# Performance work log

Measured on AMD Instinct MI355X. Metric: run time of the kernel, lower is better.

Reference implementation:

```python
import jax, jax.numpy as jnp
import numpy as np

B_, L, S_IN, S_OUT, Z_IN, Z_OUT = 2, 768, 1280, 32, 1, 32
D_INNER, D_STATE, D_CONV, DT_RANK = 64, 16, 4, 2  # expand=2 -> d_inner=64; dt_rank=ceil(32/16)=2


def setup_inputs() -> dict:
    key = jax.random.key(0)
    ks = jax.random.split(key, 12)
    p = lambda i, shape, scale=0.02: jax.random.normal(ks[i], shape, jnp.float32) * scale
    return dict(
        s=jax.random.normal(ks[0], (B_, L, S_IN), jnp.float32),
        z=jax.random.normal(ks[1], (B_, L, L, Z_IN), jnp.float32),
        s_proj_w=p(2, (S_OUT, S_IN)), s_proj_b=jnp.zeros((S_OUT,), jnp.float32),
        z_proj_w=p(3, (Z_OUT, Z_IN)), z_proj_b=jnp.zeros((Z_OUT,), jnp.float32),
        in_proj_w=p(4, (2 * D_INNER, S_OUT)),
        conv_w=p(5, (D_INNER, D_CONV)), conv_b=jnp.zeros((D_INNER,), jnp.float32),
        x_proj_w=p(6, (DT_RANK + 2 * D_STATE, D_INNER)),
        dt_proj_w=p(7, (D_INNER, DT_RANK)), dt_proj_b=p(8, (D_INNER,), 1.0),
        A_log=jnp.log(jnp.broadcast_to(jnp.arange(1, D_STATE + 1, dtype=jnp.float32), (D_INNER, D_STATE))),
        D=jnp.ones((D_INNER,), jnp.float32),
        out_proj_w=p(9, (S_OUT, D_INNER)),
    )


def mamba(u, in_proj_w, conv_w, conv_b, x_proj_w, dt_proj_w, dt_proj_b, A_log, D, out_proj_w):
    # u: [b, l, d_model]
    b, l, _ = u.shape
    xz = u @ in_proj_w.T                      # [b, l, 2*d_inner]
    x, gate = jnp.split(xz, 2, axis=-1)
    # causal depthwise conv1d, kernel D_CONV, then SiLU
    xp = jnp.pad(x, ((0, 0), (D_CONV - 1, 0), (0, 0)))
    x = sum(xp[:, k:k + l, :] * conv_w[:, k] for k in range(D_CONV)) + conv_b
    x = jax.nn.silu(x)
    x_dbl = x @ x_proj_w.T                    # [b, l, dt_rank + 2*d_state]
    dt, Bm, Cm = jnp.split(x_dbl, [DT_RANK, DT_RANK + D_STATE], axis=-1)
    dt = jax.nn.softplus(dt @ dt_proj_w.T + dt_proj_b)   # [b, l, d_inner]
    A = -jnp.exp(A_log)                       # [d_inner, d_state]
    dA = jnp.exp(dt[..., None] * A)           # [b, l, d, n]
    dBu = dt[..., None] * Bm[:, :, None, :] * x[..., None]  # [b, l, d, n]

    def step(h, ins):
        dA_t, dBu_t, C_t = ins
        h = dA_t * h + dBu_t                  # [b, d, n]
        return h, jnp.einsum('bdn,bn->bd', h, C_t)

    h0 = jnp.zeros((b, D_INNER, D_STATE), u.dtype)
    _, ys = jax.lax.scan(step, h0, (jnp.swapaxes(dA, 0, 1), jnp.swapaxes(dBu, 0, 1), jnp.swapaxes(Cm, 0, 1)))
    y = jnp.swapaxes(ys, 0, 1) + x * D        # D skip connection
    y = y * jax.nn.silu(gate)                 # gated output
    return y @ out_proj_w.T                   # [b, l, d_model]


def reference(s, z, s_proj_w, s_proj_b, z_proj_w, z_proj_b, in_proj_w, conv_w, conv_b,
              x_proj_w, dt_proj_w, dt_proj_b, A_log, D, out_proj_w):
    s_prime = s @ s_proj_w.T + s_proj_b                       # [b, l, 32]
    s_prime = mamba(s_prime, in_proj_w, conv_w, conv_b, x_proj_w,
                    dt_proj_w, dt_proj_b, A_log, D, out_proj_w)
    z_prime = z @ z_proj_w.T + z_proj_b                       # [b, l, l, 32]
    z_prime = z_prime + jnp.einsum('bsf,btf->bstf', s_prime, s_prime)
    return (s_prime, z_prime)
```

## Files before the change

### kernel.cpp

```cpp
#include <hip/hip_runtime.h>
#include <math.h>

#define B_     2
#define L_     768
#define SIN_   1280
#define SOUT_  32
#define DI_    64
#define DST_   16
#define DCONV_ 4
#define DTR_   2
#define NCH    48
#define CH     16


__global__ __launch_bounds__(256) void k_sproj(
    const float* __restrict__ s, const float* __restrict__ spw,
    const float* __restrict__ spb, const float* __restrict__ ipw,
    float* __restrict__ xz)
{
    __shared__ float srow[4][SIN_];
    __shared__ float w2[128 * 33];
    __shared__ float u[4][SOUT_];
    const int tid = threadIdx.x;
    const int row0 = blockIdx.x * 4;

    for (int r = 0; r < 4; ++r) {
        const float4* src = (const float4*)(s + (long)(row0 + r) * SIN_);
        for (int i = tid; i < SIN_ / 4; i += 256)
            ((float4*)srow[r])[i] = src[i];
    }
    for (int i = tid; i < 128 * 32; i += 256)
        w2[(i >> 5) * 33 + (i & 31)] = ipw[i];
    __syncthreads();

    const int f = tid >> 3;
    const int c = tid & 7;
    float p0 = 0.f, p1 = 0.f, p2 = 0.f, p3 = 0.f;
    const float* wrow = spw + (long)f * SIN_;
    for (int k = c; k < SIN_; k += 8) {
        float w = wrow[k];
        p0 += srow[0][k] * w; p1 += srow[1][k] * w;
        p2 += srow[2][k] * w; p3 += srow[3][k] * w;
    }
    #pragma unroll
    for (int m = 1; m <= 4; m <<= 1) {
        p0 += __shfl_xor(p0, m); p1 += __shfl_xor(p1, m);
        p2 += __shfl_xor(p2, m); p3 += __shfl_xor(p3, m);
    }
    if (c == 0) {
        float b = spb[f];
        u[0][f] = p0 + b; u[1][f] = p1 + b;
        u[2][f] = p2 + b; u[3][f] = p3 + b;
    }
    __syncthreads();

    const int j  = tid & 127;
    const int rh = tid >> 7;
    #pragma unroll
    for (int rp = 0; rp < 2; ++rp) {
        int r = rp * 2 + rh;
        float acc = 0.f;
        const float* wj = &w2[j * 33];
        #pragma unroll
        for (int k = 0; k < SOUT_; ++k) acc += u[r][k] * wj[k];
        xz[(long)(row0 + r) * 128 + j] = acc;
    }
}

__global__ __launch_bounds__(256) void k_pre(
    const float* __restrict__ xz, const float* __restrict__ convw,
    const float* __restrict__ convb, const float* __restrict__ xpw,
    const float* __restrict__ dtw, const float* __restrict__ dtb,
    float* __restrict__ xs_out, float* __restrict__ dtf,
    float* __restrict__ dtx, float* __restrict__ Bws, float* __restrict__ Cws)
{
    const int row0 = blockIdx.x * 4;
    const int tid = threadIdx.x;
    const int r = tid >> 6, d = tid & 63;
    const int row = row0 + r;
    const int b = row / L_, l = row - b * L_;
    __shared__ float sxpw[64][34];
    __shared__ float sdtw[128];
    __shared__ float sxs[4][DI_];
    __shared__ float sxd[4][34];

    for (int i = tid; i < 34 * 64; i += 256) {
        int j = i >> 6, k = i & 63;
        sxpw[k][j] = xpw[i];
    }
    if (tid < 128) sdtw[tid] = dtw[tid];

    float xc = convb[d];
    #pragma unroll
    for (int k = 0; k < DCONV_; ++k) {
        int ls = l + k - (DCONV_ - 1);
        if (ls >= 0) xc = fmaf(xz[(long)(b * L_ + ls) * 128 + d], convw[d * 4 + k], xc);
    }
    float xsv = xc / (1.f + expf(-xc));
    sxs[r][d] = xsv;
    xs_out[(long)row * DI_ + d] = xsv;
    __syncthreads();

    if (d < DTR_ + 2 * DST_) {
        float acc = 0.f;
        #pragma unroll
        for (int k = 0; k < 64; ++k) acc = fmaf(sxs[r][k], sxpw[k][d], acc);
        sxd[r][d] = acc;
    }
    __syncthreads();

    if (d < DST_) {
        Bws[(long)row * DST_ + d] = sxd[r][DTR_ + d];
        Cws[(long)row * DST_ + d] = sxd[r][DTR_ + DST_ + d];
    }
    float dtv = fmaf(sxd[r][0], sdtw[d * 2], fmaf(sxd[r][1], sdtw[d * 2 + 1], dtb[d]));
    dtv = dtv > 20.f ? dtv : log1pf(expf(dtv));
    dtf[(long)row * DI_ + d] = dtv;
    dtx[(long)row * DI_ + d] = dtv * xsv;
}

__global__ __launch_bounds__(256) void k_scan_p1(
    const float* __restrict__ dtf, const float* __restrict__ dtx,
    const float* __restrict__ Bws, const float* __restrict__ Alog,
    float* __restrict__ Pst, float* __restrict__ Lst)
{
    const int blk = blockIdx.x;
    const int dq  = blk & 3;
    const int bc  = blk >> 2;
    const int b   = bc / NCH, c = bc - b * NCH;
    const int tid = threadIdx.x;
    const int dl  = tid >> 4, n = tid & 15;
    const int d   = dq * 16 + dl;
    const long base = (long)b * L_ + c * CH;

    __shared__ float sB[CH][16];
    __shared__ float sdt[CH][16];
    __shared__ float sdx[CH][16];

    if (tid < 64) ((float4*)sB)[tid] = ((const float4*)(Bws + base * DST_))[tid];
    {
        int l = tid >> 4, j = tid & 15;
        sdt[l][j] = dtf[(base + l) * DI_ + dq * 16 + j];
        sdx[l][j] = dtx[(base + l) * DI_ + dq * 16 + j];
    }
    float A2 = -expf(Alog[d * DST_ + n]) * 1.44269504088896f;
    float P = 1.f, hl = 0.f;
    __syncthreads();

    #pragma unroll
    for (int l = 0; l < CH; ++l) {
        float a = exp2f(sdt[l][dl] * A2);
        P *= a;
        hl = fmaf(a, hl, sdx[l][dl] * sB[l][n]);
    }
    long o = (long)bc * 1024 + dq * 256 + tid;
    Pst[o] = P;
    Lst[o] = hl;
}

__global__ __launch_bounds__(256) void k_scan_p2(
    const float* __restrict__ Pst, const float* __restrict__ Lst,
    float* __restrict__ Hst)
{
    const int idx = blockIdx.x * 256 + threadIdx.x;
    const int b = idx >> 10, e = idx & 1023;
    float H = 0.f;
    #pragma unroll 8
    for (int c = 0; c < NCH; ++c) {
        long o = ((long)(b * NCH + c)) * 1024 + e;
        Hst[o] = H;
        H = fmaf(Pst[o], H, Lst[o]);
    }
}

__global__ __launch_bounds__(1024) void k_back(
    const float* __restrict__ dtf, const float* __restrict__ dtx,
    const float* __restrict__ Bws, const float* __restrict__ Cws,
    const float* __restrict__ Alog, const float* __restrict__ Hst,
    const float* __restrict__ xs, const float* __restrict__ xz,
    const float* __restrict__ Dv, const float* __restrict__ opw,
    float* __restrict__ sp)
{
    const int bc  = blockIdx.x;
    const int b   = bc / NCH, c = bc - b * NCH;
    const int tid = threadIdx.x;
    const long base = (long)b * L_ + c * CH;

    __shared__ float sB[CH][16], sC[CH][16];
    __shared__ float sdt[CH][64], sdx[CH][64];
    __shared__ float sy[CH][65];
    __shared__ float sw[64][33];

    if (tid < 64) {
        ((float4*)sB)[tid] = ((const float4*)(Bws + base * DST_))[tid];
        ((float4*)sC)[tid] = ((const float4*)(Cws + base * DST_))[tid];
    }
    {
        int l = tid >> 6, dd = tid & 63;
        sdt[l][dd] = dtf[(base + l) * DI_ + dd];
        sdx[l][dd] = dtx[(base + l) * DI_ + dd];
    }
    if (tid < SOUT_ * DI_) sw[tid & 63][tid >> 6] = opw[tid];

    const int d = tid >> 4, n = tid & 15;
    float A2 = -expf(Alog[d * DST_ + n]) * 1.44269504088896f;
    float h = Hst[(long)bc * 1024 + tid];
    __syncthreads();

    #pragma unroll
    for (int l = 0; l < CH; ++l) {
        float a = exp2f(sdt[l][d] * A2);
        h = fmaf(a, h, sdx[l][d] * sB[l][n]);
        float y = h * sC[l][n];
        y += __shfl_xor(y, 1);
        y += __shfl_xor(y, 2);
        y += __shfl_xor(y, 4);
        y += __shfl_xor(y, 8);
        if (n == 0) sy[l][d] = y;
    }
    __syncthreads();

    {
        int r = tid >> 6, dd = tid & 63;
        float g  = xz[(base + r) * 128 + DI_ + dd];
        float yv = fmaf(xs[(base + r) * DI_ + dd], Dv[dd], sy[r][dd]);
        sy[r][dd] = yv * (g / (1.f + expf(-g)));
    }
    __syncthreads();

    if (tid < CH * SOUT_) {
        int r = tid >> 5, o = tid & 31;
        float acc = 0.f;
        #pragma unroll
        for (int k = 0; k < DI_; ++k) acc = fmaf(sy[r][k], sw[k][o], acc);
        sp[(base + r) * SOUT_ + o] = acc;
    }
}

__global__ __launch_bounds__(256) void k_z(
    const float* __restrict__ z, const float* __restrict__ zw,
    const float* __restrict__ zb, const float* __restrict__ sp,
    float* __restrict__ zout)
{
    const int idx = blockIdx.x * 256 + threadIdx.x;
    const int bs  = idx / 6144;
    const int rem = idx - bs * 6144;
    const int t   = rem >> 3;
    const int f4  = rem & 7;
    const int b   = bs / L_;

    float zval = z[(long)bs * L_ + t];
    float4 w4 = ((const float4*)zw)[f4];
    float4 b4 = ((const float4*)zb)[f4];
    float4 ss = ((const float4*)sp)[bs * 8 + f4];
    float4 st = ((const float4*)sp)[(b * L_ + t) * 8 + f4];
    float4 o;
    o.x = zval * w4.x + b4.x + ss.x * st.x;
    o.y = zval * w4.y + b4.y + ss.y * st.y;
    o.z = zval * w4.z + b4.z + ss.z * st.z;
    o.w = zval * w4.w + b4.w + ss.w * st.w;
    ((float4*)zout)[(long)idx] = o;
}

extern "C" void kernel_launch(void* const* d_in, const int* in_sizes, int n_in,
                              void* d_out, int out_size, void* d_ws, size_t ws_size,
                              hipStream_t stream) {
    const float* s     = (const float*)d_in[0];
    const float* z     = (const float*)d_in[1];
    const float* spw   = (const float*)d_in[2];
    const float* spb   = (const float*)d_in[3];
    const float* zw    = (const float*)d_in[4];
    const float* zb    = (const float*)d_in[5];
    const float* ipw   = (const float*)d_in[6];
    const float* convw = (const float*)d_in[7];
    const float* convb = (const float*)d_in[8];
    const float* xpw   = (const float*)d_in[9];
    const float* dtw   = (const float*)d_in[10];
    const float* dtb   = (const float*)d_in[11];
    const float* Alog  = (const float*)d_in[12];
    const float* Dv    = (const float*)d_in[13];
    const float* opw   = (const float*)d_in[14];

    float* out = (float*)d_out;
    float* ws  = (float*)d_ws;
    float* xz  = ws;
    float* xs  = ws + 196608;
    float* dtf = ws + 294912;
    float* dtx = ws + 393216;
    float* Bws = ws + 491520;
    float* Cws = ws + 516096;
    float* Pst = ws + 540672;
    float* Lst = ws + 638976;
    float* Hst = ws + 737280;

    float* sp   = out;
    float* zout = out + 49152;

    k_sproj  <<<(B_ * L_) / 4, 256, 0, stream>>>(s, spw, spb, ipw, xz);
    k_pre    <<<(B_ * L_) / 4, 256, 0, stream>>>(xz, convw, convb, xpw, dtw, dtb,
                                                 xs, dtf, dtx, Bws, Cws);
    k_scan_p1<<<B_ * NCH * 4, 256, 0, stream>>>(dtf, dtx, Bws, Alog, Pst, Lst);
    k_scan_p2<<<8, 256, 0, stream>>>(Pst, Lst, Hst);
    k_back   <<<B_ * NCH, 1024, 0, stream>>>(dtf, dtx, Bws, Cws, Alog, Hst,
                                             xs, xz, Dv, opw, sp);
    k_z      <<<(B_ * L_ * L_ * 8) / 256, 256, 0, stream>>>(z, zw, zb, sp, zout);
}
```

Baseline: 260.8 us.

## Fuse chunk scan into pre kernel and drop scan pass-two kernel

Chunk-local scan summaries are now computed inside the pre-processing kernel, which works per chunk of 8 timesteps. The separate cross-chunk prefix kernel is removed: each backward block rebuilds its starting state by serially folding all earlier chunk summaries. The dtx buffer is dropped and recomputed from dt and x, and the s-projection uses 2 rows per block with float4 loads. This cuts two launches and some global traffic, at the cost of redundant prefix work that grows with chunk index (up to 95 steps of dependent loads per thread).

After: 258.3 us. Within noise of the previous version (-1.0%).

```diff
diff --git a/kernel.cpp b/kernel.cpp
--- a/kernel.cpp
+++ b/kernel.cpp
@@ -9,8 +9,8 @@
 #define DST_   16
 #define DCONV_ 4
 #define DTR_   2
-#define NCH    48
-#define CH     16
+#define NCH    96
+#define CH     8
 
 
 __global__ __launch_bounds__(256) void k_sproj(
@@ -18,13 +18,13 @@
     const float* __restrict__ spb, const float* __restrict__ ipw,
     float* __restrict__ xz)
 {
-    __shared__ float srow[4][SIN_];
+    __shared__ float srow[2][SIN_];
     __shared__ float w2[128 * 33];
-    __shared__ float u[4][SOUT_];
+    __shared__ float u[2][SOUT_];
     const int tid = threadIdx.x;
-    const int row0 = blockIdx.x * 4;
-
-    for (int r = 0; r < 4; ++r) {
+    const int row0 = blockIdx.x * 2;
+
+    for (int r = 0; r < 2; ++r) {
         const float4* src = (const float4*)(s + (long)(row0 + r) * SIN_);
         for (int i = tid; i < SIN_ / 4; i += 256)
             ((float4*)srow[r])[i] = src[i];
@@ -35,182 +35,182 @@
 
     const int f = tid >> 3;
     const int c = tid & 7;
-    float p0 = 0.f, p1 = 0.f, p2 = 0.f, p3 = 0.f;
-    const float* wrow = spw + (long)f * SIN_;
-    for (int k = c; k < SIN_; k += 8) {
-        float w = wrow[k];
-        p0 += srow[0][k] * w; p1 += srow[1][k] * w;
-        p2 += srow[2][k] * w; p3 += srow[3][k] * w;
+    float p0 = 0.f, p1 = 0.f;
+    const float4* w4p = (const float4*)(spw + (long)f * SIN_);
+    const float4* a0p = (const float4*)srow[0];
+    const float4* a1p = (const float4*)srow[1];
+    for (int k4 = c; k4 < SIN_ / 4; k4 += 8) {
+        float4 w  = w4p[k4];
+        float4 a0 = a0p[k4];
+        float4 a1 = a1p[k4];
+        p0 = fmaf(a0.x, w.x, fmaf(a0.y, w.y, fmaf(a0.z, w.z, fmaf(a0.w, w.w, p0))));
+        p1 = fmaf(a1.x, w.x, fmaf(a1.y, w.y, fmaf(a1.z, w.z, fmaf(a1.w, w.w, p1))));
     }
     #pragma unroll
     for (int m = 1; m <= 4; m <<= 1) {
-        p0 += __shfl_xor(p0, m); p1 += __shfl_xor(p1, m);
-        p2 += __shfl_xor(p2, m); p3 += __shfl_xor(p3, m);
+        p0 += __shfl_xor(p0, m);
+        p1 += __shfl_xor(p1, m);
     }
     if (c == 0) {
-        float b = spb[f];
-        u[0][f] = p0 + b; u[1][f] = p1 + b;
-        u[2][f] = p2 + b; u[3][f] = p3 + b;
-    }
-    __syncthreads();
-
-    const int j  = tid & 127;
-    const int rh = tid >> 7;
-    #pragma unroll
-    for (int rp = 0; rp < 2; ++rp) {
-        int r = rp * 2 + rh;
-        float acc = 0.f;
-        const float* wj = &w2[j * 33];
-        #pragma unroll
-        for (int k = 0; k < SOUT_; ++k) acc += u[r][k] * wj[k];
-        xz[(long)(row0 + r) * 128 + j] = acc;
-    }
+        float bb = spb[f];
+        u[0][f] = p0 + bb;
+        u[1][f] = p1 + bb;
+    }
+    __syncthreads();
+
+    const int j = tid & 127;
+    const int r = tid >> 7;
+    float acc = 0.f;
+    const float* wj = &w2[j * 33];
+    #pragma unroll
+    for (int k = 0; k < SOUT_; ++k) acc += u[r][k] * wj[k];
+    xz[(long)(row0 + r) * 128 + j] = acc;
 }
 
 __global__ __launch_bounds__(256) void k_pre(
     const float* __restrict__ xz, const float* __restrict__ convw,
     const float* __restrict__ convb, const float* __restrict__ xpw,
     const float* __restrict__ dtw, const float* __restrict__ dtb,
-    float* __restrict__ xs_out, float* __restrict__ dtf,
-    float* __restrict__ dtx, float* __restrict__ Bws, float* __restrict__ Cws)
+    const float* __restrict__ Alog,
+    float* __restrict__ xs_out, float* __restrict__ dtf_out,
+    float* __restrict__ Bws, float* __restrict__ Cws,
+    float* __restrict__ Pst, float* __restrict__ Lst)
 {
-    const int row0 = blockIdx.x * 4;
+    const int bc = blockIdx.x;
+    const int b  = bc / NCH, c = bc - b * NCH;
+    const int l0 = c * CH;
+    const long rbase = (long)b * L_ + l0;
     const int tid = threadIdx.x;
-    const int r = tid >> 6, d = tid & 63;
-    const int row = row0 + r;
-    const int b = row / L_, l = row - b * L_;
+
     __shared__ float sxpw[64][34];
     __shared__ float sdtw[128];
-    __shared__ float sxs[4][DI_];
-    __shared__ float sxd[4][34];
-
-    for (int i = tid; i < 34 * 64; i += 256) {
-        int j = i >> 6, k = i & 63;
-        sxpw[k][j] = xpw[i];
-    }
+    __shared__ float sxs[CH][DI_];
+    __shared__ float sxd[CH][34];
+    __shared__ float sdt[CH][DI_];
+    __shared__ float sdx[CH][DI_];
+
+    for (int i = tid; i < 34 * 64; i += 256)
+        sxpw[i & 63][i >> 6] = xpw[i];
     if (tid < 128) sdtw[tid] = dtw[tid];
 
-    float xc = convb[d];
-    #pragma unroll
-    for (int k = 0; k < DCONV_; ++k) {
-        int ls = l + k - (DCONV_ - 1);
-        if (ls >= 0) xc = fmaf(xz[(long)(b * L_ + ls) * 128 + d], convw[d * 4 + k], xc);
-    }
-    float xsv = xc / (1.f + expf(-xc));
-    sxs[r][d] = xsv;
-    xs_out[(long)row * DI_ + d] = xsv;
-    __syncthreads();
-
-    if (d < DTR_ + 2 * DST_) {
+    for (int it = tid; it < CH * DI_; it += 256) {
+        int r = it >> 6, d = it & 63;
+        int l = l0 + r;
+        float xc = convb[d];
+        #pragma unroll
+        for (int k = 0; k < DCONV_; ++k) {
+            int ls = l + k - (DCONV_ - 1);
+            if (ls >= 0) xc = fmaf(xz[(long)(b * L_ + ls) * 128 + d], convw[d * 4 + k], xc);
+        }
+        float xv = xc / (1.f + expf(-xc));
+        sxs[r][d] = xv;
+        xs_out[(rbase + r) * DI_ + d] = xv;
+    }
+    __syncthreads();
+
+    for (int it = tid; it < CH * 34; it += 256) {
+        int r = it / 34, o = it - r * 34;
         float acc = 0.f;
         #pragma unroll
-        for (int k = 0; k < 64; ++k) acc = fmaf(sxs[r][k], sxpw[k][d], acc);
-        sxd[r][d] = acc;
-    }
-    __syncthreads();
-
-    if (d < DST_) {
-        Bws[(long)row * DST_ + d] = sxd[r][DTR_ + d];
-        Cws[(long)row * DST_ + d] = sxd[r][DTR_ + DST_ + d];
-    }
-    float dtv = fmaf(sxd[r][0], sdtw[d * 2], fmaf(sxd[r][1], sdtw[d * 2 + 1], dtb[d]));
-    dtv = dtv > 20.f ? dtv : log1pf(expf(dtv));
-    dtf[(long)row * DI_ + d] = dtv;
-    dtx[(long)row * DI_ + d] = dtv * xsv;
-}
-
-__global__ __launch_bounds__(256) void k_scan_p1(
-    const float* __restrict__ dtf, const float* __restrict__ dtx,
-    const float* __restrict__ Bws, const float* __restrict__ Alog,
-    float* __restrict__ Pst, float* __restrict__ Lst)
-{
-    const int blk = blockIdx.x;
-    const int dq  = blk & 3;
-    const int bc  = blk >> 2;
-    const int b   = bc / NCH, c = bc - b * NCH;
-    const int tid = threadIdx.x;
-    const int dl  = tid >> 4, n = tid & 15;
-    const int d   = dq * 16 + dl;
-    const long base = (long)b * L_ + c * CH;
-
-    __shared__ float sB[CH][16];
-    __shared__ float sdt[CH][16];
-    __shared__ float sdx[CH][16];
-
-    if (tid < 64) ((float4*)sB)[tid] = ((const float4*)(Bws + base * DST_))[tid];
-    {
-        int l = tid >> 4, j = tid & 15;
-        sdt[l][j] = dtf[(base + l) * DI_ + dq * 16 + j];
-        sdx[l][j] = dtx[(base + l) * DI_ + dq * 16 + j];
-    }
-    float A2 = -expf(Alog[d * DST_ + n]) * 1.44269504088896f;
-    float P = 1.f, hl = 0.f;
-    __syncthreads();
-
+        for (int k = 0; k < DI_; ++k) acc = fmaf(sxs[r][k], sxpw[k][o], acc);
+        sxd[r][o] = acc;
+    }
+    __syncthreads();
+
+    for (int it = tid; it < CH * DI_; it += 256) {
+        int r = it >> 6, d = it & 63;
+        float dtv = fmaf(sxd[r][0], sdtw[2 * d], fmaf(sxd[r][1], sdtw[2 * d + 1], dtb[d]));
+        dtv = dtv > 20.f ? dtv : log1pf(expf(dtv));
+        sdt[r][d] = dtv;
+        sdx[r][d] = dtv * sxs[r][d];
+        dtf_out[(rbase + r) * DI_ + d] = dtv;
+    }
+    if (tid < CH * DST_) {
+        int r = tid >> 4, n = tid & 15;
+        Bws[(rbase + r) * DST_ + n] = sxd[r][DTR_ + n];
+        Cws[(rbase + r) * DST_ + n] = sxd[r][DTR_ + DST_ + n];
+    }
+    __syncthreads();
+
+    const int n = tid & 15, g = tid >> 4;
+    float P[4], hl[4], A2[4];
+    #pragma unroll
+    for (int q = 0; q < 4; ++q) {
+        int d = g + 16 * q;
+        A2[q] = -expf(Alog[d * DST_ + n]) * 1.44269504088896f;
+        P[q] = 1.f; hl[q] = 0.f;
+    }
     #pragma unroll
     for (int l = 0; l < CH; ++l) {
-        float a = exp2f(sdt[l][dl] * A2);
-        P *= a;
-        hl = fmaf(a, hl, sdx[l][dl] * sB[l][n]);
-    }
-    long o = (long)bc * 1024 + dq * 256 + tid;
-    Pst[o] = P;
-    Lst[o] = hl;
-}
-
-__global__ __launch_bounds__(256) void k_scan_p2(
-    const float* __restrict__ Pst, const float* __restrict__ Lst,
-    float* __restrict__ Hst)
-{
-    const int idx = blockIdx.x * 256 + threadIdx.x;
-    const int b = idx >> 10, e = idx & 1023;
-    float H = 0.f;
-    #pragma unroll 8
-    for (int c = 0; c < NCH; ++c) {
-        long o = ((long)(b * NCH + c)) * 1024 + e;
-        Hst[o] = H;
-        H = fmaf(Pst[o], H, Lst[o]);
+        float bv = sxd[l][DTR_ + n];
+        #pragma unroll
+        for (int q = 0; q < 4; ++q) {
+            int d = g + 16 * q;
+            float a = exp2f(sdt[l][d] * A2[q]);
+            P[q] *= a;
+            hl[q] = fmaf(a, hl[q], sdx[l][d] * bv);
+        }
+    }
+    const long o0 = (long)bc * 1024 + g * 16 + n;
+    #pragma unroll
+    for (int q = 0; q < 4; ++q) {
+        Pst[o0 + 256 * q] = P[q];
+        Lst[o0 + 256 * q] = hl[q];
     }
 }
 
 __global__ __launch_bounds__(1024) void k_back(
-    const float* __restrict__ dtf, const float* __restrict__ dtx,
+    const float* __restrict__ dtf, const float* __restrict__ xs,
     const float* __restrict__ Bws, const float* __restrict__ Cws,
-    const float* __restrict__ Alog, const float* __restrict__ Hst,
-    const float* __restrict__ xs, const float* __restrict__ xz,
+    const float* __restrict__ Alog, const float* __restrict__ Pst,
+    const float* __restrict__ Lst, const float* __restrict__ xz,
     const float* __restrict__ Dv, const float* __restrict__ opw,
     float* __restrict__ sp)
 {
-    const int bc  = blockIdx.x;
-    const int b   = bc / NCH, c = bc - b * NCH;
+    const int bc = blockIdx.x;
+    const int b  = bc / NCH, c = bc - b * NCH;
+    const int l0 = c * CH;
+    const long rbase = (long)b * L_ + l0;
     const int tid = threadIdx.x;
-    const long base = (long)b * L_ + c * CH;
-
-    __shared__ float sB[CH][16], sC[CH][16];
-    __shared__ float sdt[CH][64], sdx[CH][64];
+
+    __shared__ float sB[CH][DST_], sC[CH][DST_];
+    __shared__ float sdt[CH][DI_], sxsS[CH][DI_];
     __shared__ float sy[CH][65];
     __shared__ float sw[64][33];
 
-    if (tid < 64) {
-        ((float4*)sB)[tid] = ((const float4*)(Bws + base * DST_))[tid];
-        ((float4*)sC)[tid] = ((const float4*)(Cws + base * DST_))[tid];
-    }
+    if (tid < CH * DI_) {
+        sdt[tid >> 6][tid & 63] = dtf[rbase * DI_ + tid];
+    } else {
+        int t = tid - CH * DI_;
+        sxsS[t >> 6][t & 63] = xs[rbase * DI_ + t];
+    }
+    if (tid < CH * DST_) {
+        sB[tid >> 4][tid & 15] = Bws[rbase * DST_ + tid];
+    } else if (tid < 2 * CH * DST_) {
+        int t = tid - CH * DST_;
+        sC[t >> 4][t & 15] = Cws[rbase * DST_ + t];
+    }
+    for (int i = tid; i < SOUT_ * DI_; i += 1024)
+        sw[i & 63][i >> 6] = opw[i];
+
+    float h = 0.f;
     {
-        int l = tid >> 6, dd = tid & 63;
-        sdt[l][dd] = dtf[(base + l) * DI_ + dd];
-        sdx[l][dd] = dtx[(base + l) * DI_ + dd];
-    }
-    if (tid < SOUT_ * DI_) sw[tid & 63][tid >> 6] = opw[tid];
-
+        const long ebase = (long)b * NCH * 1024 + tid;
+        #pragma unroll 4
+        for (int c2 = 0; c2 < c; ++c2) {
+            long o = ebase + (long)c2 * 1024;
+            h = fmaf(Pst[o], h, Lst[o]);
+        }
+    }
     const int d = tid >> 4, n = tid & 15;
     float A2 = -expf(Alog[d * DST_ + n]) * 1.44269504088896f;
-    float h = Hst[(long)bc * 1024 + tid];
     __syncthreads();
 
     #pragma unroll
     for (int l = 0; l < CH; ++l) {
-        float a = exp2f(sdt[l][d] * A2);
-        h = fmaf(a, h, sdx[l][d] * sB[l][n]);
+        float dtv = sdt[l][d];
+        float a = exp2f(dtv * A2);
+        h = fmaf(a, h, dtv * sxsS[l][d] * sB[l][n]);
         float y = h * sC[l][n];
         y += __shfl_xor(y, 1);
         y += __shfl_xor(y, 2);
@@ -220,10 +220,10 @@
     }
     __syncthreads();
 
-    {
+    if (tid < CH * DI_) {
         int r = tid >> 6, dd = tid & 63;
-        float g  = xz[(base + r) * 128 + DI_ + dd];
-        float yv = fmaf(xs[(base + r) * DI_ + dd], Dv[dd], sy[r][dd]);
+        float g  = xz[(rbase + r) * 128 + DI_ + dd];
+        float yv = fmaf(sxsS[r][dd], Dv[dd], sy[r][dd]);
         sy[r][dd] = yv * (g / (1.f + expf(-g)));
     }
     __syncthreads();
@@ -233,7 +233,7 @@
         float acc = 0.f;
         #pragma unroll
         for (int k = 0; k < DI_; ++k) acc = fmaf(sy[r][k], sw[k][o], acc);
-        sp[(base + r) * SOUT_ + o] = acc;
+        sp[(rbase + r) * SOUT_ + o] = acc;
     }
 }
 
@@ -286,22 +286,18 @@
     float* xz  = ws;
     float* xs  = ws + 196608;
     float* dtf = ws + 294912;
-    float* dtx = ws + 393216;
-    float* Bws = ws + 491520;
-    float* Cws = ws + 516096;
-    float* Pst = ws + 540672;
+    float* Bws = ws + 393216;
+    float* Cws = ws + 417792;
+    float* Pst = ws + 442368;
     float* Lst = ws + 638976;
-    float* Hst = ws + 737280;
 
     float* sp   = out;
     float* zout = out + 49152;
 
-    k_sproj  <<<(B_ * L_) / 4, 256, 0, stream>>>(s, spw, spb, ipw, xz);
-    k_pre    <<<(B_ * L_) / 4, 256, 0, stream>>>(xz, convw, convb, xpw, dtw, dtb,
-                                                 xs, dtf, dtx, Bws, Cws);
-    k_scan_p1<<<B_ * NCH * 4, 256, 0, stream>>>(dtf, dtx, Bws, Alog, Pst, Lst);
-    k_scan_p2<<<8, 256, 0, stream>>>(Pst, Lst, Hst);
-    k_back   <<<B_ * NCH, 1024, 0, stream>>>(dtf, dtx, Bws, Cws, Alog, Hst,
-                                             xs, xz, Dv, opw, sp);
-    k_z      <<<(B_ * L_ * L_ * 8) / 256, 256, 0, stream>>>(z, zw, zb, sp, zout);
-}
+    k_sproj<<<(B_ * L_) / 2, 256, 0, stream>>>(s, spw, spb, ipw, xz);
+    k_pre  <<<B_ * NCH, 256, 0, stream>>>(xz, convw, convb, xpw, dtw, dtb, Alog,
+                                          xs, dtf, Bws, Cws, Pst, Lst);
+    k_back <<<B_ * NCH, 1024, 0, stream>>>(dtf, xs, Bws, Cws, Alog, Pst, Lst,
+                                           xz, Dv, opw, sp);
+    k_z    <<<(B_ * L_ * L_ * 8) / 256, 256, 0, stream>>>(z, zw, zb, sp, zout);
+}
```
